# Optimization experiments

Hardware: AMD Instinct MI355X
Metric: run time of the kernel (lower is better)

The kernel has to match this reference:

```python
import jax, jax.numpy as jnp
import numpy as np

IOU_THRESHOLDS = (0.5, 0.75)
B, N, G = 256, 4000, 50


def _iou(amin, amax, bmin, bmax):
    # broadcasted temporal IoU: anchors [N,1] vs boxes [1,G] -> [N,G]
    inter = jnp.maximum(jnp.minimum(amax, bmax) - jnp.maximum(amin, bmin), 0.0)
    union = (amax - amin) + (bmax - bmin) - inter
    return inter / union


def _greedy_tp(segments, gts, thr):
    # segments: [N,2], gts: [G,2]. Replicates AP.get_values greedy matching:
    # for each label (in order), claim the first (lowest-index) unused proposal
    # whose IoU > thr. Final used-mask == is_TP.
    ious = _iou(segments[:, 0:1], segments[:, 1:2], gts[None, :, 0], gts[None, :, 1])  # [N,G]
    pot = ious > thr
    n = segments.shape[0]

    def step(used, col):  # col: [N] bool, candidates for this label
        cand = col & ~used
        idx = jnp.argmax(cand)  # first True (argmax of bool is first max)
        used = jnp.where(jnp.any(cand), used.at[idx].set(True), used)
        return used, None

    used, _ = jax.lax.scan(step, jnp.zeros((n,), jnp.bool_), pot.T)
    return used  # [N] bool


def _ap_for_threshold(scores, segments, labels, thr):
    is_tp = jax.vmap(lambda s, g: _greedy_tp(s, g, thr))(segments, labels)  # [B,N]
    conf = scores.reshape(-1)                       # [B*N]
    tp = is_tp.reshape(-1).astype(jnp.float32)
    order = jnp.argsort(-conf)                      # sort by confidence, descending
    tp = tp[order]
    n_labels = labels.shape[0] * labels.shape[1]
    m = tp.shape[0]
    acc_tp = jnp.cumsum(tp)
    precision = acc_tp / (jnp.arange(m, dtype=jnp.float32) + 1.0)
    recall = acc_tp / jnp.float32(n_labels)
    # curve = [[1,0]] then (recall, precision) reversed; AP = sum(|dx| * cummax(y)[:-1])
    x = jnp.concatenate([jnp.ones((1,), jnp.float32), recall[::-1]])
    y = jnp.concatenate([jnp.zeros((1,), jnp.float32), precision[::-1]])
    y_max = jax.lax.cummax(y, axis=0)
    x_diff = jnp.abs(jnp.diff(x))
    return jnp.sum(x_diff * y_max[:-1])


def setup_inputs() -> dict:
    key = jax.random.key(0)
    k1, k2, k3, k4, k5 = jax.random.split(key, 5)
    scores = jax.random.uniform(k1, (B, N), dtype=jnp.float32)
    p_start = jax.random.uniform(k2, (B, N), dtype=jnp.float32) * 0.9
    p_len = jax.random.uniform(k3, (B, N), dtype=jnp.float32) * 0.1 + 0.005
    segments = jnp.stack([p_start, p_start + p_len], axis=-1)  # [B,N,2], start<end
    g_start = jax.random.uniform(k4, (B, G), dtype=jnp.float32) * 0.9
    g_len = jax.random.uniform(k5, (B, G), dtype=jnp.float32) * 0.1 + 0.005
    labels = jnp.stack([g_start, g_start + g_len], axis=-1)    # [B,G,2]
    return {"scores": scores, "segments": segments, "labels": labels}


def reference(scores, segments, labels):
    # returns AP at each IoU threshold, shape [len(IOU_THRESHOLDS)]
    return jnp.stack([_ap_for_threshold(scores, segments, labels, t) for t in IOU_THRESHOLDS])
```

## Files before the change

### kernel.cpp

```cpp
#include <hip/hip_runtime.h>


#define B_ 256
#define N_ 4000
#define G_ 50
#define M_ (B_ * N_)
#define NL_ (B_ * G_)
#define NBKT 1024
#define KP 16
#define TILE (NL_ / KP)

#define M0_ 0x1.000001p-1
#define M1_ 0x1.800001p-1

__device__ __forceinline__ unsigned bucket_of(float c) {
    unsigned b = (unsigned)(c * 1024.0f);
    return b > (NBKT - 1) ? (NBKT - 1) : b;
}

__global__ __launch_bounds__(1024) void tp_kernel(
    const float* __restrict__ seg,
    const float* __restrict__ gts,
    const float* __restrict__ conf,
    int* __restrict__ tpIdx,
    int* __restrict__ cnt,
    unsigned short* __restrict__ pbh)
{
    const int tid  = threadIdx.x;
    const int lane = tid & 63;
    const int wv   = tid >> 6;
    const int b    = blockIdx.x;

    __shared__ float2 gtl[G_];
    __shared__ unsigned long long cand[2][G_][64];
    __shared__ unsigned hls[NBKT];
    __shared__ int lcnt[2];

    if (tid < NBKT) hls[tid] = 0u;
    if (tid < G_) gtl[tid] = ((const float2*)gts)[b * G_ + tid];
    if (tid < 2) lcnt[tid] = 0;
    __syncthreads();

    const float* cb = conf + (size_t)b * N_;
    #pragma unroll
    for (int s = 0; s < 4; ++s) {
        int n = s * 1024 + tid;
        if (n < N_) atomicAdd(&hls[bucket_of(cb[n])], 1u);
    }

    const float2* sb = (const float2*)(seg + (size_t)b * (N_ * 2));
    float pmin[4], pmax[4], plen[4];
    #pragma unroll
    for (int s = 0; s < 4; ++s) {
        int n = s * 1024 + tid;
        if (n < N_) { float2 v = sb[n]; pmin[s] = v.x; pmax[s] = v.y; }
        else { pmin[s] = 1e9f; pmax[s] = 1e9f; }
        plen[s] = pmax[s] - pmin[s];
    }
    for (int g = 0; g < G_; ++g) {
        float2 gt = gtl[g];
        float glen = gt.y - gt.x;
        unsigned long long m0[4], m1[4];
        #pragma unroll
        for (int s = 0; s < 4; ++s) {
            float inter = fmaxf(fminf(pmax[s], gt.y) - fmaxf(pmin[s], gt.x), 0.0f);
            float uni = plen[s] + glen - inter;
            double di = (double)inter;
            double du = (double)uni;
            m0[s] = __ballot(di > M0_ * du);
            m1[s] = __ballot(di > M1_ * du);
        }
        if (lane == 0) {
            #pragma unroll
            for (int s = 0; s < 4; ++s) {
                cand[0][g][s * 16 + wv] = m0[s];
                cand[1][g][s * 16 + wv] = m1[s];
            }
        }
    }
    __syncthreads();

    if (tid < NBKT) pbh[(size_t)b * NBKT + tid] = (unsigned short)hls[tid];

    if (wv < 2) {
        const int thr_i = wv;
        unsigned long long used = 0ull;
        for (int g = 0; g < G_; ++g) {
            unsigned long long c = cand[thr_i][g][lane] & ~used;
            unsigned long long ball = __ballot(c != 0ull);
            if (ball) {
                int fl = __ffsll(ball) - 1;
                if (lane == fl) used |= (c & (0ull - c));
            }
        }
        int cpop = __popcll(used);
        if (cpop) {
            int j = atomicAdd(&lcnt[thr_i], cpop);
            unsigned long long u = used;
            while (u) {
                int bit = __ffsll(u) - 1;
                u &= u - 1;
                tpIdx[thr_i * NL_ + b * G_ + j++] = b * N_ + lane * 64 + bit;
            }
        }
    }
    __syncthreads();
    if (tid < 2) cnt[tid * B_ + b] = lcnt[tid];
}

__global__ __launch_bounds__(256) void s1_kernel(
    unsigned short* __restrict__ pbh,
    unsigned* __restrict__ total)
{
    int bin = blockIdx.x * 256 + threadIdx.x;
    unsigned run = 0;
    for (int b = 0; b < B_; ++b) {
        size_t o = (size_t)b * NBKT + bin;
        unsigned v = pbh[o];
        pbh[o] = (unsigned short)run;
        run += v;
    }
    total[bin] = run;
}

__global__ __launch_bounds__(1024) void s2_kernel(
    const unsigned* __restrict__ total, unsigned* __restrict__ binStart)
{
    __shared__ unsigned part[1024];
    int t = threadIdx.x;
    part[t] = total[t];
    __syncthreads();
    for (int off = 1; off < 1024; off <<= 1) {
        unsigned add = (t >= off) ? part[t - off] : 0u;
        unsigned v = part[t];
        __syncthreads();
        part[t] = v + add;
        __syncthreads();
    }
    binStart[t] = (t == 0) ? 0u : part[t - 1];
}

__global__ __launch_bounds__(1024) void scatter_kernel(
    const float* __restrict__ conf,
    const unsigned short* __restrict__ pbh,
    const unsigned* __restrict__ binStart,
    float2* __restrict__ sPair)
{
    __shared__ unsigned baseB[NBKT];
    __shared__ unsigned lofs[NBKT];
    const int tid = threadIdx.x;
    const int b = blockIdx.x;
    if (tid < NBKT) {
        baseB[tid] = binStart[tid] + pbh[(size_t)b * NBKT + tid];
        lofs[tid] = 0u;
    }
    __syncthreads();
    const float* cb = conf + (size_t)b * N_;
    #pragma unroll
    for (int s = 0; s < 4; ++s) {
        int n = s * 1024 + tid;
        if (n < N_) {
            float c = cb[n];
            unsigned bin = bucket_of(c);
            unsigned lo = atomicAdd(&lofs[bin], 1u);
            sPair[baseB[bin] + lo] = make_float2(c, __uint_as_float((unsigned)(b * N_ + n)));
        }
    }
}

__global__ __launch_bounds__(256) void rank_kernel(
    const float* __restrict__ conf,
    const int* __restrict__ tpIdx,
    const int* __restrict__ cnt,
    const unsigned* __restrict__ total,
    const unsigned* __restrict__ binStart,
    const float2* __restrict__ sPair,
    int* __restrict__ tpRank)
{
    const int lane = threadIdx.x & 63;
    const int w = (blockIdx.x << 2) | (threadIdx.x >> 6);
    if (w >= 2 * NL_) return;
    const int thr_i = w / NL_;
    const int t = w - thr_i * NL_;
    const int batch = t / G_;
    const int j = t - batch * G_;

    if (j < cnt[thr_i * B_ + batch]) {
        int e = tpIdx[thr_i * NL_ + t];
        float c = conf[e];
        unsigned bin = bucket_of(c);
        unsigned lo = binStart[bin], n = total[bin];
        int r = M_ - (int)lo - (int)n;
        for (unsigned base = 0; base < n; base += 64) {
            unsigned k = base + lane;
            bool pred = false;
            if (k < n) {
                float2 p = sPair[lo + k];
                unsigned si = __float_as_uint(p.y);
                pred = (p.x > c) || (p.x == c && si < (unsigned)e);
            }
            r += (int)__popcll(__ballot(pred));
        }
        if (lane == 0) tpRank[thr_i * NL_ + t] = r;
    } else {
        if (lane == 0) tpRank[thr_i * NL_ + t] = M_ + t;
    }
}

__global__ __launch_bounds__(256) void pos1_kernel(
    const int* __restrict__ tpRank,
    int* __restrict__ pcount)
{
    __shared__ alignas(16) int tile[TILE];
    const int k = blockIdx.y, thr_i = blockIdx.z;
    const int* base = tpRank + thr_i * NL_;
    for (int i = threadIdx.x; i < TILE; i += 256)
        tile[i] = base[k * TILE + i];
    __syncthreads();

    const int t0 = blockIdx.x * 1024 + threadIdx.x;
    int r[4], c[4] = {0, 0, 0, 0};
    #pragma unroll
    for (int j = 0; j < 4; ++j) {
        int t = t0 + j * 256;
        r[j] = (t < NL_) ? base[t] : -1;
    }
    const int4* l4 = (const int4*)tile;
    #pragma unroll 4
    for (int i = 0; i < TILE / 4; ++i) {
        int4 v = l4[i];
        #pragma unroll
        for (int j = 0; j < 4; ++j)
            c[j] += (v.x < r[j]) + (v.y < r[j]) + (v.z < r[j]) + (v.w < r[j]);
    }
    #pragma unroll
    for (int j = 0; j < 4; ++j) {
        int t = t0 + j * 256;
        if (t < NL_) pcount[(thr_i * KP + k) * NL_ + t] = c[j];
    }
}

__global__ __launch_bounds__(256) void pos2_kernel(
    const int* __restrict__ tpRank,
    const int* __restrict__ pcount,
    int* __restrict__ sortedRank)
{
    int gt = blockIdx.x * 256 + threadIdx.x;
    int thr_i = gt / NL_;
    int t = gt - thr_i * NL_;
    int p = 0;
    #pragma unroll
    for (int k = 0; k < KP; ++k)
        p += pcount[(thr_i * KP + k) * NL_ + t];
    sortedRank[thr_i * NL_ + p] = tpRank[thr_i * NL_ + t];
}

__global__ __launch_bounds__(1024) void ap_kernel(const int* __restrict__ sortedRank,
                                                  float* __restrict__ out)
{
    const int C = 13;
    int thr_i = blockIdx.x;
    int t = threadIdx.x;
    const int* sr = sortedRank + thr_i * NL_;

    float pr[C]; int rk[C];
    #pragma unroll
    for (int k = 0; k < C; ++k) {
        int i = t * C + k;
        rk[k] = (i < NL_) ? sr[i] : 0x7FFFFFFF;
        pr[k] = (rk[k] < M_) ? (float)(i + 1) / (float)(rk[k] + 1) : -1.0f;
    }
    float suf[C];
    float run = -1.0f;
    #pragma unroll
    for (int k = C - 1; k >= 0; --k) { run = fmaxf(run, pr[k]); suf[k] = run; }

    __shared__ float cmax[1024];
    cmax[t] = run;
    __syncthreads();
    for (int off = 1; off < 1024; off <<= 1) {
        float v = cmax[t];
        float o = (t + off < 1024) ? cmax[t + off] : -1.0f;
        __syncthreads();
        cmax[t] = fmaxf(v, o);
        __syncthreads();
    }
    float follow = (t + 1 < 1024) ? cmax[t + 1] : -1.0f;

    double acc = 0.0;
    #pragma unroll
    for (int k = 0; k < C; ++k) {
        int i = t * C + k;
        if (rk[k] >= 1 && rk[k] < M_) {
            float smax = fmaxf(suf[k], follow);
            float rhi = (float)(i + 1) / 12800.0f;
            float rlo = (float)i / 12800.0f;
            acc += (double)((rhi - rlo) * smax);
        }
    }
    __shared__ double red[1024];
    red[t] = acc;
    __syncthreads();
    for (int off = 512; off >= 1; off >>= 1) {
        if (t < off) red[t] += red[t + off];
        __syncthreads();
    }
    if (t == 0) out[thr_i] = (float)red[0];
}

extern "C" void kernel_launch(void* const* d_in, const int* in_sizes, int n_in,
                              void* d_out, int out_size, void* d_ws, size_t ws_size,
                              hipStream_t stream) {
    const float* scores = (const float*)d_in[0];
    const float* seg    = (const float*)d_in[1];
    const float* gts    = (const float*)d_in[2];
    float* out = (float*)d_out;

    char* p = (char*)d_ws;
    int*            cnt        = (int*)p;             p += 4096;
    int*            tpIdx      = (int*)p;             p += 2 * NL_ * 4;
    int*            tpRank     = (int*)p;             p += 2 * NL_ * 4;
    int*            sortedRank = (int*)p;             p += 2 * NL_ * 4;
    unsigned*       total      = (unsigned*)p;        p += NBKT * 4;
    unsigned*       binStart   = (unsigned*)p;        p += NBKT * 4;
    unsigned short* pbh        = (unsigned short*)p;  p += (size_t)B_ * NBKT * 2;
    float2*         sPair      = (float2*)p;          p += (size_t)M_ * 8;
    int*            pcount     = (int*)sPair;
    (void)ws_size; (void)in_sizes; (void)n_in; (void)out_size;

    tp_kernel<<<B_, 1024, 0, stream>>>(seg, gts, scores, tpIdx, cnt, pbh);
    s1_kernel<<<NBKT / 256, 256, 0, stream>>>(pbh, total);
    s2_kernel<<<1, 1024, 0, stream>>>(total, binStart);
    scatter_kernel<<<B_, 1024, 0, stream>>>(scores, pbh, binStart, sPair);
    rank_kernel<<<(2 * NL_ + 3) / 4, 256, 0, stream>>>(scores, tpIdx, cnt,
                                                       total, binStart, sPair, tpRank);
    pos1_kernel<<<dim3(13, KP, 2), 256, 0, stream>>>(tpRank, pcount);
    pos2_kernel<<<2 * NL_ / 256, 256, 0, stream>>>(tpRank, pcount, sortedRank);
    ap_kernel<<<2, 1024, 0, stream>>>(sortedRank, out);
}
```

Baseline: 191.4 us.

## Parallelize per-bin column scan, pack sort keys into u64, fuse pos2 into ap kernel

The per-bin prefix over 256 batches was a serial loop on 1024 threads; it now runs as 1024 blocks each doing a shared-memory parallel scan over batches. Score/index pairs are packed into a single 64-bit key so the rank comparison becomes one unsigned compare. The pos2 scatter is folded into ap_kernel via a shared-memory sorted array, dropping one launch and a global round trip. The fused kernel does the pcount reduction on only 2 blocks and uses more shared memory (~100KB), which could limit it.

Result: no change. 192.2 us (+0.4%).

```diff
diff --git a/kernel.cpp b/kernel.cpp
--- a/kernel.cpp
+++ b/kernel.cpp
@@ -13,6 +13,8 @@
 #define M0_ 0x1.000001p-1
 #define M1_ 0x1.800001p-1
 
+typedef unsigned long long u64;
+
 __device__ __forceinline__ unsigned bucket_of(float c) {
     unsigned b = (unsigned)(c * 1024.0f);
     return b > (NBKT - 1) ? (NBKT - 1) : b;
@@ -32,7 +34,7 @@
     const int b    = blockIdx.x;
 
     __shared__ float2 gtl[G_];
-    __shared__ unsigned long long cand[2][G_][64];
+    __shared__ u64 cand[2][G_][64];
     __shared__ unsigned hls[NBKT];
     __shared__ int lcnt[2];
 
@@ -60,7 +62,7 @@
     for (int g = 0; g < G_; ++g) {
         float2 gt = gtl[g];
         float glen = gt.y - gt.x;
-        unsigned long long m0[4], m1[4];
+        u64 m0[4], m1[4];
         #pragma unroll
         for (int s = 0; s < 4; ++s) {
             float inter = fmaxf(fminf(pmax[s], gt.y) - fmaxf(pmin[s], gt.x), 0.0f);
@@ -84,10 +86,10 @@
 
     if (wv < 2) {
         const int thr_i = wv;
-        unsigned long long used = 0ull;
+        u64 used = 0ull;
         for (int g = 0; g < G_; ++g) {
-            unsigned long long c = cand[thr_i][g][lane] & ~used;
-            unsigned long long ball = __ballot(c != 0ull);
+            u64 c = cand[thr_i][g][lane] & ~used;
+            u64 ball = __ballot(c != 0ull);
             if (ball) {
                 int fl = __ffsll(ball) - 1;
                 if (lane == fl) used |= (c & (0ull - c));
@@ -96,7 +98,7 @@
         int cpop = __popcll(used);
         if (cpop) {
             int j = atomicAdd(&lcnt[thr_i], cpop);
-            unsigned long long u = used;
+            u64 u = used;
             while (u) {
                 int bit = __ffsll(u) - 1;
                 u &= u - 1;
@@ -112,15 +114,20 @@
     unsigned short* __restrict__ pbh,
     unsigned* __restrict__ total)
 {
-    int bin = blockIdx.x * 256 + threadIdx.x;
-    unsigned run = 0;
-    for (int b = 0; b < B_; ++b) {
-        size_t o = (size_t)b * NBKT + bin;
-        unsigned v = pbh[o];
-        pbh[o] = (unsigned short)run;
-        run += v;
-    }
-    total[bin] = run;
+    __shared__ unsigned sc[256];
+    const int bin = blockIdx.x;
+    const int b = threadIdx.x;
+    unsigned v = pbh[(size_t)b * NBKT + bin];
+    sc[b] = v;
+    __syncthreads();
+    for (int off = 1; off < 256; off <<= 1) {
+        unsigned add = (b >= off) ? sc[b - off] : 0u;
+        __syncthreads();
+        sc[b] += add;
+        __syncthreads();
+    }
+    pbh[(size_t)b * NBKT + bin] = (unsigned short)(sc[b] - v);
+    if (b == 255) total[bin] = sc[255];
 }
 
 __global__ __launch_bounds__(1024) void s2_kernel(
@@ -132,9 +139,8 @@
     __syncthreads();
     for (int off = 1; off < 1024; off <<= 1) {
         unsigned add = (t >= off) ? part[t - off] : 0u;
-        unsigned v = part[t];
-        __syncthreads();
-        part[t] = v + add;
+        __syncthreads();
+        part[t] += add;
         __syncthreads();
     }
     binStart[t] = (t == 0) ? 0u : part[t - 1];
@@ -144,7 +150,7 @@
     const float* __restrict__ conf,
     const unsigned short* __restrict__ pbh,
     const unsigned* __restrict__ binStart,
-    float2* __restrict__ sPair)
+    u64* __restrict__ sKey)
 {
     __shared__ unsigned baseB[NBKT];
     __shared__ unsigned lofs[NBKT];
@@ -163,7 +169,8 @@
             float c = cb[n];
             unsigned bin = bucket_of(c);
             unsigned lo = atomicAdd(&lofs[bin], 1u);
-            sPair[baseB[bin] + lo] = make_float2(c, __uint_as_float((unsigned)(b * N_ + n)));
+            unsigned idx = (unsigned)(b * N_ + n);
+            sKey[baseB[bin] + lo] = ((u64)__float_as_uint(c) << 32) | (u64)(0xFFFFFFFFu - idx);
         }
     }
 }
@@ -174,7 +181,7 @@
     const int* __restrict__ cnt,
     const unsigned* __restrict__ total,
     const unsigned* __restrict__ binStart,
-    const float2* __restrict__ sPair,
+    const u64* __restrict__ sKey,
     int* __restrict__ tpRank)
 {
     const int lane = threadIdx.x & 63;
@@ -188,17 +195,13 @@
     if (j < cnt[thr_i * B_ + batch]) {
         int e = tpIdx[thr_i * NL_ + t];
         float c = conf[e];
+        u64 keyE = ((u64)__float_as_uint(c) << 32) | (u64)(0xFFFFFFFFu - (unsigned)e);
         unsigned bin = bucket_of(c);
         unsigned lo = binStart[bin], n = total[bin];
         int r = M_ - (int)lo - (int)n;
         for (unsigned base = 0; base < n; base += 64) {
             unsigned k = base + lane;
-            bool pred = false;
-            if (k < n) {
-                float2 p = sPair[lo + k];
-                unsigned si = __float_as_uint(p.y);
-                pred = (p.x > c) || (p.x == c && si < (unsigned)e);
-            }
+            bool pred = (k < n) && (sKey[lo + k] > keyE);
             r += (int)__popcll(__ballot(pred));
         }
         if (lane == 0) tpRank[thr_i * NL_ + t] = r;
@@ -240,28 +243,30 @@
     }
 }
 
-__global__ __launch_bounds__(256) void pos2_kernel(
+__global__ __launch_bounds__(1024) void ap_kernel(
     const int* __restrict__ tpRank,
     const int* __restrict__ pcount,
-    int* __restrict__ sortedRank)
-{
-    int gt = blockIdx.x * 256 + threadIdx.x;
-    int thr_i = gt / NL_;
-    int t = gt - thr_i * NL_;
-    int p = 0;
-    #pragma unroll
-    for (int k = 0; k < KP; ++k)
-        p += pcount[(thr_i * KP + k) * NL_ + t];
-    sortedRank[thr_i * NL_ + p] = tpRank[thr_i * NL_ + t];
-}
-
-__global__ __launch_bounds__(1024) void ap_kernel(const int* __restrict__ sortedRank,
-                                                  float* __restrict__ out)
+    float* __restrict__ out)
 {
     const int C = 13;
+    __shared__ int sr[NL_];
+    __shared__ float cmax[1024];
+    __shared__ double red[1024];
     int thr_i = blockIdx.x;
     int t = threadIdx.x;
-    const int* sr = sortedRank + thr_i * NL_;
+
+    #pragma unroll
+    for (int j = 0; j < C; ++j) {
+        int tt = t + j * 1024;
+        if (tt < NL_) {
+            int p = 0;
+            #pragma unroll
+            for (int k = 0; k < KP; ++k)
+                p += pcount[(thr_i * KP + k) * NL_ + tt];
+            sr[p] = tpRank[thr_i * NL_ + tt];
+        }
+    }
+    __syncthreads();
 
     float pr[C]; int rk[C];
     #pragma unroll
@@ -275,7 +280,6 @@
     #pragma unroll
     for (int k = C - 1; k >= 0; --k) { run = fmaxf(run, pr[k]); suf[k] = run; }
 
-    __shared__ float cmax[1024];
     cmax[t] = run;
     __syncthreads();
     for (int off = 1; off < 1024; off <<= 1) {
@@ -298,7 +302,6 @@
             acc += (double)((rhi - rlo) * smax);
         }
     }
-    __shared__ double red[1024];
     red[t] = acc;
     __syncthreads();
     for (int off = 512; off >= 1; off >>= 1) {
@@ -320,21 +323,19 @@
     int*            cnt        = (int*)p;             p += 4096;
     int*            tpIdx      = (int*)p;             p += 2 * NL_ * 4;
     int*            tpRank     = (int*)p;             p += 2 * NL_ * 4;
-    int*            sortedRank = (int*)p;             p += 2 * NL_ * 4;
     unsigned*       total      = (unsigned*)p;        p += NBKT * 4;
     unsigned*       binStart   = (unsigned*)p;        p += NBKT * 4;
     unsigned short* pbh        = (unsigned short*)p;  p += (size_t)B_ * NBKT * 2;
-    float2*         sPair      = (float2*)p;          p += (size_t)M_ * 8;
-    int*            pcount     = (int*)sPair;
+    u64*            sKey       = (u64*)p;             p += (size_t)M_ * 8;
+    int*            pcount     = (int*)sKey;
     (void)ws_size; (void)in_sizes; (void)n_in; (void)out_size;
 
     tp_kernel<<<B_, 1024, 0, stream>>>(seg, gts, scores, tpIdx, cnt, pbh);
-    s1_kernel<<<NBKT / 256, 256, 0, stream>>>(pbh, total);
+    s1_kernel<<<NBKT, 256, 0, stream>>>(pbh, total);
     s2_kernel<<<1, 1024, 0, stream>>>(total, binStart);
-    scatter_kernel<<<B_, 1024, 0, stream>>>(scores, pbh, binStart, sPair);
+    scatter_kernel<<<B_, 1024, 0, stream>>>(scores, pbh, binStart, sKey);
     rank_kernel<<<(2 * NL_ + 3) / 4, 256, 0, stream>>>(scores, tpIdx, cnt,
-                                                       total, binStart, sPair, tpRank);
+                                                       total, binStart, sKey, tpRank);
     pos1_kernel<<<dim3(13, KP, 2), 256, 0, stream>>>(tpRank, pcount);
-    pos2_kernel<<<2 * NL_ / 256, 256, 0, stream>>>(tpRank, pcount, sortedRank);
-    ap_kernel<<<2, 1024, 0, stream>>>(sortedRank, out);
-}
+    ap_kernel<<<2, 1024, 0, stream>>>(tpRank, pcount, out);
+}
```
